# Kernel tuning notes

Hardware: AMD Instinct MI355X
Metric: run time of the kernel (lower is better)

The kernel has to match this reference:

```python
import jax, jax.numpy as jnp
import numpy as np

N_NODES = 100000
N_EDGES = 800000
N_GRAPHS = 256
IN_C = 96
HID = 96
OUT_C = 16


def setup_inputs() -> dict:
    key = jax.random.key(0)
    ks = jax.random.split(key, 10)
    x = jax.random.normal(ks[0], (N_NODES, IN_C), dtype=jnp.float32)
    edge_index = jax.random.randint(ks[1], (2, N_EDGES), 0, N_NODES, dtype=jnp.int64)
    batch = jnp.sort(jax.random.randint(ks[2], (N_NODES,), 0, N_GRAPHS, dtype=jnp.int64))
    def glorot(k, fan_in, fan_out):
        s = np.sqrt(6.0 / (fan_in + fan_out)).astype(np.float32)
        return jax.random.uniform(k, (fan_in, fan_out), minval=-s, maxval=s, dtype=jnp.float32)
    W1 = glorot(ks[3], IN_C, HID)
    W2 = glorot(ks[4], HID, HID)
    W3 = glorot(ks[5], HID, HID)
    Wlin = glorot(ks[6], HID, OUT_C)
    b1 = jnp.zeros((HID,), dtype=jnp.float32)
    b2 = jnp.zeros((HID,), dtype=jnp.float32)
    b3 = jnp.zeros((HID,), dtype=jnp.float32)
    return {"x": x, "edge_index": edge_index, "batch": batch,
            "W1": W1, "b1": b1, "W2": W2, "b2": b2, "W3": W3, "b3": b3, "Wlin": Wlin}


def _gcn_conv(x, W, b, src, dst):
    # PyG GCNConv(normalize=True): add self-loops, deg includes self-loop,
    # norm_ij = deg_i^{-1/2} * deg_j^{-1/2}; linear (no bias) then scatter-add; bias after.
    n = x.shape[0]
    deg = jnp.zeros((n,), dtype=x.dtype).at[dst].add(1.0) + 1.0  # +1 self-loop
    dinv = jax.lax.rsqrt(deg)
    h = x @ W                                   # [N, H]
    coef = dinv[src] * dinv[dst]                # [E]
    msg = h[src] * coef[:, None]                # [E, H] gather
    agg = jax.ops.segment_sum(msg, dst, num_segments=n)  # scatter-add
    agg = agg + h * (dinv * dinv)[:, None]      # self-loop contribution
    return agg + b


def reference(x, edge_index, batch, W1, b1, W2, b2, W3, b3, Wlin):
    src, dst = edge_index[0], edge_index[1]
    h = jax.nn.relu(_gcn_conv(x, W1, b1, src, dst))
    h = jax.nn.relu(_gcn_conv(h, W2, b2, src, dst))
    h = _gcn_conv(h, W3, b3, src, dst)
    # global mean pool over graphs
    sums = jax.ops.segment_sum(h, batch, num_segments=N_GRAPHS)
    counts = jax.ops.segment_sum(jnp.ones((h.shape[0],), dtype=h.dtype), batch, num_segments=N_GRAPHS)
    pooled = sums / jnp.maximum(counts, 1.0)[:, None]
    return pooled @ Wlin
```

## Files before the change

### kernel.cpp

```cpp
#include <hip/hip_runtime.h>

#define NN 100000
#define NE 800000
#define NG 256
#define CH 96
#define OC 16
#define NBLK 391
#define TM 128
#define WPAD 104

typedef __attribute__((ext_vector_type(8))) short bf16x8;
typedef __attribute__((ext_vector_type(4))) float f32x4;

__global__ __launch_bounds__(256) void k_hist(const int* __restrict__ dst,
                                              int* __restrict__ cnt,
                                              int* __restrict__ slot) {
    int e = blockIdx.x * 256 + threadIdx.x;
    slot[e] = atomicAdd(&cnt[dst[e]], 1);
}

__global__ __launch_bounds__(256) void k_scan1(const int* __restrict__ cnt,
                                               int* __restrict__ off,
                                               int* __restrict__ bsum) {
    __shared__ int sh[256];
    int t = threadIdx.x;
    int i = blockIdx.x * 256 + t;
    int v = (i < NN) ? cnt[i] : 0;
    sh[t] = v;
    __syncthreads();
    for (int d = 1; d < 256; d <<= 1) {
        int x = (t >= d) ? sh[t - d] : 0;
        __syncthreads();
        sh[t] += x;
        __syncthreads();
    }
    if (i < NN) off[i] = sh[t] - v;
    if (t == 255) bsum[blockIdx.x] = sh[255];
}

__global__ __launch_bounds__(512) void k_scan2(int* __restrict__ bsum,
                                               int* __restrict__ boff) {
    __shared__ int sh[512];
    int t = threadIdx.x;
    int v = (t < NBLK) ? bsum[t] : 0;
    sh[t] = v;
    __syncthreads();
    for (int d = 1; d < 512; d <<= 1) {
        int x = (t >= d) ? sh[t - d] : 0;
        __syncthreads();
        sh[t] += x;
        __syncthreads();
    }
    if (t < NBLK) boff[t] = sh[t] - v;
}

__global__ __launch_bounds__(256) void k_scan3(const int* __restrict__ cnt,
                                               int* __restrict__ off,
                                               const int* __restrict__ boff,
                                               float* __restrict__ dinv,
                                               const int* __restrict__ batch,
                                               int* __restrict__ goff) {
    int i = blockIdx.x * 256 + threadIdx.x;
    if (i >= NN) return;
    off[i] += boff[i >> 8];
    dinv[i] = rsqrtf((float)cnt[i] + 1.0f);
    int b = batch[i];
    int bp = (i > 0) ? batch[i - 1] : -1;
    for (int g = bp + 1; g <= b; g++) goff[g] = i;
    if (i == NN - 1)
        for (int g = b + 1; g <= NG; g++) goff[g] = NN;
}

__global__ __launch_bounds__(256) void k_build(const int* __restrict__ src,
                                               const int* __restrict__ dst,
                                               const int* __restrict__ off,
                                               const int* __restrict__ slot,
                                               const float* __restrict__ dinv,
                                               float2* __restrict__ packed) {
    int e = blockIdx.x * 256 + threadIdx.x;
    int s = src[e];
    int d = dst[e];
    packed[off[d] + slot[e]] = make_float2(__int_as_float(s), dinv[s] * dinv[d]);
}

__device__ __forceinline__ unsigned short f2bf(float x) {
    unsigned u = __float_as_uint(x);
    return (unsigned short)((u + 0x7fffu + ((u >> 16) & 1u)) >> 16);
}
__device__ __forceinline__ float bf2f(unsigned short h) {
    return __uint_as_float(((unsigned)h) << 16);
}

__device__ __forceinline__ void split8(const float4 a, const float4 b,
                                       bf16x8& hi, bf16x8& lo) {
    float v[8] = {a.x, a.y, a.z, a.w, b.x, b.y, b.z, b.w};
#pragma unroll
    for (int j = 0; j < 8; j++) {
        unsigned short h = f2bf(v[j]);
        hi[j] = (short)h;
        lo[j] = (short)f2bf(v[j] - bf2f(h));
    }
}

__global__ __launch_bounds__(256) void k_gemm96(const float* __restrict__ X,
                                                const float* __restrict__ W,
                                                unsigned short* __restrict__ H) {
    __shared__ unsigned short WtHi[CH * WPAD];
    __shared__ unsigned short WtLo[CH * WPAD];

    const int tid = threadIdx.x;
    const int n0 = blockIdx.x * TM;

    {
        const float4* W4 = reinterpret_cast<const float4*>(W);
#pragma unroll
        for (int i = 0; i < 9; i++) {
            int f4 = tid * 9 + i;
            int k = f4 / 24;
            int nn = (f4 - k * 24) * 4;
            float4 v = W4[f4];
            float vv[4] = {v.x, v.y, v.z, v.w};
#pragma unroll
            for (int e = 0; e < 4; e++) {
                unsigned short h = f2bf(vv[e]);
                WtHi[(nn + e) * WPAD + k] = h;
                WtLo[(nn + e) * WPAD + k] = f2bf(vv[e] - bf2f(h));
            }
        }
    }
    __syncthreads();

    const int lane = tid & 63;
    const int wave = tid >> 6;
    const int lrow = lane & 15;
    const int quad = lane >> 4;

    const float4* X4 = reinterpret_cast<const float4*>(X);

    f32x4 acc[2][6];
#pragma unroll
    for (int rt = 0; rt < 2; rt++)
#pragma unroll
        for (int ct = 0; ct < 6; ct++) acc[rt][ct] = (f32x4){0.f, 0.f, 0.f, 0.f};

    int arow[2];
#pragma unroll
    for (int rt = 0; rt < 2; rt++)
        arow[rt] = min(n0 + (wave * 2 + rt) * 16 + lrow, NN - 1);

#pragma unroll
    for (int kc = 0; kc < 3; kc++) {
        bf16x8 ahi[2], alo[2];
#pragma unroll
        for (int rt = 0; rt < 2; rt++) {
            int fo = (arow[rt] * CH + kc * 32 + quad * 8) >> 2;
            split8(X4[fo], X4[fo + 1], ahi[rt], alo[rt]);
        }
#pragma unroll
        for (int ct = 0; ct < 6; ct++) {
            int bo = (ct * 16 + lrow) * WPAD + kc * 32 + quad * 8;
            bf16x8 bhi = *reinterpret_cast<const bf16x8*>(&WtHi[bo]);
            bf16x8 blo = *reinterpret_cast<const bf16x8*>(&WtLo[bo]);
#pragma unroll
            for (int rt = 0; rt < 2; rt++) {
                acc[rt][ct] = __builtin_amdgcn_mfma_f32_16x16x32_bf16(
                    alo[rt], bhi, acc[rt][ct], 0, 0, 0);
                acc[rt][ct] = __builtin_amdgcn_mfma_f32_16x16x32_bf16(
                    ahi[rt], blo, acc[rt][ct], 0, 0, 0);
                acc[rt][ct] = __builtin_amdgcn_mfma_f32_16x16x32_bf16(
                    ahi[rt], bhi, acc[rt][ct], 0, 0, 0);
            }
        }
    }

#pragma unroll
    for (int rt = 0; rt < 2; rt++) {
        int rbase = n0 + (wave * 2 + rt) * 16 + quad * 4;
#pragma unroll
        for (int ct = 0; ct < 6; ct++) {
            int col = ct * 16 + lrow;
#pragma unroll
            for (int r = 0; r < 4; r++) {
                int row = rbase + r;
                if (row < NN) H[(size_t)row * CH + col] = f2bf(acc[rt][ct][r]);
            }
        }
    }
}

__device__ __forceinline__ float4 us4_to_f4(ushort4 u) {
    return make_float4(bf2f(u.x), bf2f(u.y), bf2f(u.z), bf2f(u.w));
}

template <bool RELU>
__global__ __launch_bounds__(256) void k_aggregate(const int* __restrict__ off,
                                                   const float2* __restrict__ packed,
                                                   const float* __restrict__ dinv,
                                                   const float* __restrict__ bias,
                                                   const unsigned short* __restrict__ H,
                                                   float* __restrict__ B) {
    int idx = blockIdx.x * 256 + threadIdx.x;
    int n = idx / 24;
    int c4 = idx - n * 24;
    int e0 = off[n];
    int e1 = (n + 1 < NN) ? off[n + 1] : NE;

    const ushort4* H4 = reinterpret_cast<const ushort4*>(H);
    float di = dinv[n];
    float d2 = di * di;
    float4 h = us4_to_f4(H4[(size_t)n * 24 + c4]);
    float4 bb = reinterpret_cast<const float4*>(bias)[c4];
    float4 acc = make_float4(h.x * d2 + bb.x, h.y * d2 + bb.y,
                             h.z * d2 + bb.z, h.w * d2 + bb.w);

    int e = e0;
    for (; e + 4 <= e1; e += 4) {
        float2 p0 = packed[e + 0];
        float2 p1 = packed[e + 1];
        float2 p2 = packed[e + 2];
        float2 p3 = packed[e + 3];
        float4 v0 = us4_to_f4(H4[(size_t)__float_as_int(p0.x) * 24 + c4]);
        float4 v1 = us4_to_f4(H4[(size_t)__float_as_int(p1.x) * 24 + c4]);
        float4 v2 = us4_to_f4(H4[(size_t)__float_as_int(p2.x) * 24 + c4]);
        float4 v3 = us4_to_f4(H4[(size_t)__float_as_int(p3.x) * 24 + c4]);
        acc.x += v0.x * p0.y + v1.x * p1.y + v2.x * p2.y + v3.x * p3.y;
        acc.y += v0.y * p0.y + v1.y * p1.y + v2.y * p2.y + v3.y * p3.y;
        acc.z += v0.z * p0.y + v1.z * p1.y + v2.z * p2.y + v3.z * p3.y;
        acc.w += v0.w * p0.y + v1.w * p1.y + v2.w * p2.y + v3.w * p3.y;
    }
    for (; e < e1; e++) {
        float2 pc = packed[e];
        float4 v = us4_to_f4(H4[(size_t)__float_as_int(pc.x) * 24 + c4]);
        acc.x += v.x * pc.y; acc.y += v.y * pc.y;
        acc.z += v.z * pc.y; acc.w += v.w * pc.y;
    }
    if (RELU) {
        acc.x = fmaxf(acc.x, 0.0f); acc.y = fmaxf(acc.y, 0.0f);
        acc.z = fmaxf(acc.z, 0.0f); acc.w = fmaxf(acc.w, 0.0f);
    }
    reinterpret_cast<float4*>(B)[(size_t)n * 24 + c4] = acc;
}

__global__ __launch_bounds__(384) void k_pool_linear(const int* __restrict__ goff,
                                                     const float* __restrict__ B,
                                                     const float* __restrict__ Wlin,
                                                     float* __restrict__ out) {
    __shared__ float4 sh[16][24];
    __shared__ float pooled[CH];
    int g = blockIdx.x;
    int t = threadIdx.x;
    int nl = t / 24;
    int c4 = t - nl * 24;
    int s = goff[g];
    int e = goff[g + 1];

    float4 acc = make_float4(0.f, 0.f, 0.f, 0.f);
    const float4* B4 = reinterpret_cast<const float4*>(B);
    for (int n = s + nl; n < e; n += 16) {
        float4 v = B4[(size_t)n * 24 + c4];
        acc.x += v.x; acc.y += v.y; acc.z += v.z; acc.w += v.w;
    }
    sh[nl][c4] = acc;
    __syncthreads();

    if (t < 24) {
        float4 r = make_float4(0.f, 0.f, 0.f, 0.f);
#pragma unroll
        for (int j = 0; j < 16; j++) {
            float4 v = sh[j][t];
            r.x += v.x; r.y += v.y; r.z += v.z; r.w += v.w;
        }
        float inv = 1.0f / fmaxf((float)(e - s), 1.0f);
        pooled[t * 4 + 0] = r.x * inv;
        pooled[t * 4 + 1] = r.y * inv;
        pooled[t * 4 + 2] = r.z * inv;
        pooled[t * 4 + 3] = r.w * inv;
    }
    __syncthreads();

    if (t < OC) {
        float a = 0.0f;
#pragma unroll 8
        for (int k = 0; k < CH; k++) a += pooled[k] * Wlin[k * OC + t];
        out[g * OC + t] = a;
    }
}

extern "C" void kernel_launch(void* const* d_in, const int* in_sizes, int n_in,
                              void* d_out, int out_size, void* d_ws, size_t ws_size,
                              hipStream_t stream) {
    const float* x = (const float*)d_in[0];
    const int* ei = (const int*)d_in[1];
    const int* src = ei;
    const int* dst = ei + NE;
    const int* batch = (const int*)d_in[2];
    const float* W1 = (const float*)d_in[3];
    const float* b1 = (const float*)d_in[4];
    const float* W2 = (const float*)d_in[5];
    const float* b2 = (const float*)d_in[6];
    const float* W3 = (const float*)d_in[7];
    const float* b3 = (const float*)d_in[8];
    const float* Wlin = (const float*)d_in[9];
    float* out = (float*)d_out;

    char* ws = (char*)d_ws;
    unsigned short* H = (unsigned short*)ws;  ws += (size_t)NN * CH * 2;
    float* B = (float*)ws;         ws += (size_t)NN * CH * 4;
    float2* packed = (float2*)ws;  ws += (size_t)NE * 8;
    float* dinv = (float*)ws;      ws += NN * 4;
    int* cnt = (int*)ws;           ws += NN * 4;
    int* off = (int*)ws;           ws += NN * 4;
    int* bsum = (int*)ws;          ws += 512 * 4;
    int* boff = (int*)ws;          ws += 512 * 4;
    int* goff = (int*)ws;          ws += (NG + 1) * 4;
    int* slot = (int*)B;

    hipMemsetAsync(cnt, 0, NN * 4, stream);
    k_hist<<<NE / 256, 256, 0, stream>>>(dst, cnt, slot);
    k_scan1<<<NBLK, 256, 0, stream>>>(cnt, off, bsum);
    k_scan2<<<1, 512, 0, stream>>>(bsum, boff);
    k_scan3<<<NBLK, 256, 0, stream>>>(cnt, off, boff, dinv, batch, goff);
    k_build<<<NE / 256, 256, 0, stream>>>(src, dst, off, slot, dinv, packed);

    const int gblk = (NN + TM - 1) / TM;

    k_gemm96<<<gblk, 256, 0, stream>>>(x, W1, H);
    k_aggregate<true><<<NN * 24 / 256, 256, 0, stream>>>(off, packed, dinv, b1, H, B);

    k_gemm96<<<gblk, 256, 0, stream>>>(B, W2, H);
    k_aggregate<true><<<NN * 24 / 256, 256, 0, stream>>>(off, packed, dinv, b2, H, B);

    k_gemm96<<<gblk, 256, 0, stream>>>(B, W3, H);
    k_aggregate<false><<<NN * 24 / 256, 256, 0, stream>>>(off, packed, dinv, b3, H, B);

    k_pool_linear<<<NG, 384, 0, stream>>>(goff, B, Wlin, out);
}
```

Before: 321.6 us.

## Replace scan with atomic offsets, pre-split weights once, pad edge tail loop

Replaces the three-kernel prefix scan with a single kernel that assigns per-node CSR offsets through an atomicAdd on a global counter, so segments land in arbitrary order and end offsets come from cnt. Weight bf16 hi/lo splitting and transposition move into a one-time prep kernel, and the GEMM blocks now just copy the pre-split weights into LDS, unpadded. The aggregation loop drops its scalar tail by padding the packed array and zeroing coefficients past the segment end. The cost is contended atomics in the offset kernel and edge segments that are no longer stored in node order, plus possible LDS bank conflicts from dropping the padding.

Measured after the change: 331.3 us. +3.0%, slower.

```diff
diff --git a/kernel.cpp b/kernel.cpp
--- a/kernel.cpp
+++ b/kernel.cpp
@@ -7,10 +7,30 @@
 #define OC 16
 #define NBLK 391
 #define TM 128
-#define WPAD 104
 
 typedef __attribute__((ext_vector_type(8))) short bf16x8;
 typedef __attribute__((ext_vector_type(4))) float f32x4;
+
+__device__ __forceinline__ unsigned short f2bf(float x) {
+    unsigned u = __float_as_uint(x);
+    return (unsigned short)((u + 0x7fffu + ((u >> 16) & 1u)) >> 16);
+}
+__device__ __forceinline__ float bf2f(unsigned short h) {
+    return __uint_as_float(((unsigned)h) << 16);
+}
+__device__ __forceinline__ void split8(const float4 a, const float4 b,
+                                       bf16x8& hi, bf16x8& lo) {
+    float v[8] = {a.x, a.y, a.z, a.w, b.x, b.y, b.z, b.w};
+#pragma unroll
+    for (int j = 0; j < 8; j++) {
+        unsigned short h = f2bf(v[j]);
+        hi[j] = (short)h;
+        lo[j] = (short)f2bf(v[j] - bf2f(h));
+    }
+}
+__device__ __forceinline__ float4 us4_to_f4(ushort4 u) {
+    return make_float4(bf2f(u.x), bf2f(u.y), bf2f(u.z), bf2f(u.w));
+}
 
 __global__ __launch_bounds__(256) void k_hist(const int* __restrict__ dst,
                                               int* __restrict__ cnt,
@@ -19,51 +39,17 @@
     slot[e] = atomicAdd(&cnt[dst[e]], 1);
 }
 
-__global__ __launch_bounds__(256) void k_scan1(const int* __restrict__ cnt,
-                                               int* __restrict__ off,
-                                               int* __restrict__ bsum) {
-    __shared__ int sh[256];
-    int t = threadIdx.x;
-    int i = blockIdx.x * 256 + t;
-    int v = (i < NN) ? cnt[i] : 0;
-    sh[t] = v;
-    __syncthreads();
-    for (int d = 1; d < 256; d <<= 1) {
-        int x = (t >= d) ? sh[t - d] : 0;
-        __syncthreads();
-        sh[t] += x;
-        __syncthreads();
-    }
-    if (i < NN) off[i] = sh[t] - v;
-    if (t == 255) bsum[blockIdx.x] = sh[255];
-}
-
-__global__ __launch_bounds__(512) void k_scan2(int* __restrict__ bsum,
-                                               int* __restrict__ boff) {
-    __shared__ int sh[512];
-    int t = threadIdx.x;
-    int v = (t < NBLK) ? bsum[t] : 0;
-    sh[t] = v;
-    __syncthreads();
-    for (int d = 1; d < 512; d <<= 1) {
-        int x = (t >= d) ? sh[t - d] : 0;
-        __syncthreads();
-        sh[t] += x;
-        __syncthreads();
-    }
-    if (t < NBLK) boff[t] = sh[t] - v;
-}
-
-__global__ __launch_bounds__(256) void k_scan3(const int* __restrict__ cnt,
-                                               int* __restrict__ off,
-                                               const int* __restrict__ boff,
-                                               float* __restrict__ dinv,
-                                               const int* __restrict__ batch,
-                                               int* __restrict__ goff) {
+__global__ __launch_bounds__(256) void k_offsets(const int* __restrict__ cnt,
+                                                 int* __restrict__ gtot,
+                                                 int* __restrict__ off,
+                                                 float* __restrict__ dinv,
+                                                 const int* __restrict__ batch,
+                                                 int* __restrict__ goff) {
     int i = blockIdx.x * 256 + threadIdx.x;
     if (i >= NN) return;
-    off[i] += boff[i >> 8];
-    dinv[i] = rsqrtf((float)cnt[i] + 1.0f);
+    int c = cnt[i];
+    off[i] = atomicAdd(gtot, c);
+    dinv[i] = rsqrtf((float)c + 1.0f);
     int b = batch[i];
     int bp = (i > 0) ? batch[i - 1] : -1;
     for (int g = bp + 1; g <= b; g++) goff[g] = i;
@@ -81,51 +67,46 @@
     int s = src[e];
     int d = dst[e];
     packed[off[d] + slot[e]] = make_float2(__int_as_float(s), dinv[s] * dinv[d]);
-}
-
-__device__ __forceinline__ unsigned short f2bf(float x) {
-    unsigned u = __float_as_uint(x);
-    return (unsigned short)((u + 0x7fffu + ((u >> 16) & 1u)) >> 16);
-}
-__device__ __forceinline__ float bf2f(unsigned short h) {
-    return __uint_as_float(((unsigned)h) << 16);
-}
-
-__device__ __forceinline__ void split8(const float4 a, const float4 b,
-                                       bf16x8& hi, bf16x8& lo) {
-    float v[8] = {a.x, a.y, a.z, a.w, b.x, b.y, b.z, b.w};
-#pragma unroll
-    for (int j = 0; j < 8; j++) {
-        unsigned short h = f2bf(v[j]);
-        hi[j] = (short)h;
-        lo[j] = (short)f2bf(v[j] - bf2f(h));
-    }
+    if (blockIdx.x == 0 && threadIdx.x < 8)
+        packed[NE + threadIdx.x] = make_float2(__int_as_float(0), 0.0f);
+}
+
+__global__ __launch_bounds__(256) void k_prep(const float* __restrict__ W1,
+                                              const float* __restrict__ W2,
+                                              const float* __restrict__ W3,
+                                              unsigned short* __restrict__ WH,
+                                              unsigned short* __restrict__ WL) {
+    int id = blockIdx.x * 256 + threadIdx.x;
+    if (id >= 3 * CH * CH) return;
+    int w = id / (CH * CH);
+    int r = id - w * CH * CH;
+    int k = r / CH;
+    int n = r - k * CH;
+    const float* Ws = (w == 0) ? W1 : (w == 1) ? W2 : W3;
+    float v = Ws[k * CH + n];
+    unsigned short h = f2bf(v);
+    WH[w * CH * CH + n * CH + k] = h;
+    WL[w * CH * CH + n * CH + k] = f2bf(v - bf2f(h));
 }
 
 __global__ __launch_bounds__(256) void k_gemm96(const float* __restrict__ X,
-                                                const float* __restrict__ W,
+                                                const unsigned short* __restrict__ WH,
+                                                const unsigned short* __restrict__ WL,
                                                 unsigned short* __restrict__ H) {
-    __shared__ unsigned short WtHi[CH * WPAD];
-    __shared__ unsigned short WtLo[CH * WPAD];
+    __shared__ __align__(16) unsigned short WsH[CH * CH];
+    __shared__ __align__(16) unsigned short WsL[CH * CH];
 
     const int tid = threadIdx.x;
     const int n0 = blockIdx.x * TM;
 
     {
-        const float4* W4 = reinterpret_cast<const float4*>(W);
-#pragma unroll
-        for (int i = 0; i < 9; i++) {
-            int f4 = tid * 9 + i;
-            int k = f4 / 24;
-            int nn = (f4 - k * 24) * 4;
-            float4 v = W4[f4];
-            float vv[4] = {v.x, v.y, v.z, v.w};
-#pragma unroll
-            for (int e = 0; e < 4; e++) {
-                unsigned short h = f2bf(vv[e]);
-                WtHi[(nn + e) * WPAD + k] = h;
-                WtLo[(nn + e) * WPAD + k] = f2bf(vv[e] - bf2f(h));
-            }
+        const uint4* sH = reinterpret_cast<const uint4*>(WH);
+        const uint4* sL = reinterpret_cast<const uint4*>(WL);
+        uint4* dH = reinterpret_cast<uint4*>(WsH);
+        uint4* dL = reinterpret_cast<uint4*>(WsL);
+        for (int i = tid; i < CH * CH / 8; i += 256) {
+            dH[i] = sH[i];
+            dL[i] = sL[i];
         }
     }
     __syncthreads();
@@ -158,9 +139,9 @@
         }
 #pragma unroll
         for (int ct = 0; ct < 6; ct++) {
-            int bo = (ct * 16 + lrow) * WPAD + kc * 32 + quad * 8;
-            bf16x8 bhi = *reinterpret_cast<const bf16x8*>(&WtHi[bo]);
-            bf16x8 blo = *reinterpret_cast<const bf16x8*>(&WtLo[bo]);
+            int bo = (ct * 16 + lrow) * CH + kc * 32 + quad * 8;
+            bf16x8 bhi = *reinterpret_cast<const bf16x8*>(&WsH[bo]);
+            bf16x8 blo = *reinterpret_cast<const bf16x8*>(&WsL[bo]);
 #pragma unroll
             for (int rt = 0; rt < 2; rt++) {
                 acc[rt][ct] = __builtin_amdgcn_mfma_f32_16x16x32_bf16(
@@ -188,12 +169,9 @@
     }
 }
 
-__device__ __forceinline__ float4 us4_to_f4(ushort4 u) {
-    return make_float4(bf2f(u.x), bf2f(u.y), bf2f(u.z), bf2f(u.w));
-}
-
 template <bool RELU>
 __global__ __launch_bounds__(256) void k_aggregate(const int* __restrict__ off,
+                                                   const int* __restrict__ cnt,
                                                    const float2* __restrict__ packed,
                                                    const float* __restrict__ dinv,
                                                    const float* __restrict__ bias,
@@ -203,7 +181,7 @@
     int n = idx / 24;
     int c4 = idx - n * 24;
     int e0 = off[n];
-    int e1 = (n + 1 < NN) ? off[n + 1] : NE;
+    int e1 = e0 + cnt[n];
 
     const ushort4* H4 = reinterpret_cast<const ushort4*>(H);
     float di = dinv[n];
@@ -213,26 +191,23 @@
     float4 acc = make_float4(h.x * d2 + bb.x, h.y * d2 + bb.y,
                              h.z * d2 + bb.z, h.w * d2 + bb.w);
 
-    int e = e0;
-    for (; e + 4 <= e1; e += 4) {
+    for (int e = e0; e < e1; e += 4) {
         float2 p0 = packed[e + 0];
         float2 p1 = packed[e + 1];
         float2 p2 = packed[e + 2];
         float2 p3 = packed[e + 3];
+        float c0 = p0.y;
+        float c1 = (e + 1 < e1) ? p1.y : 0.0f;
+        float c2 = (e + 2 < e1) ? p2.y : 0.0f;
+        float c3 = (e + 3 < e1) ? p3.y : 0.0f;
         float4 v0 = us4_to_f4(H4[(size_t)__float_as_int(p0.x) * 24 + c4]);
         float4 v1 = us4_to_f4(H4[(size_t)__float_as_int(p1.x) * 24 + c4]);
         float4 v2 = us4_to_f4(H4[(size_t)__float_as_int(p2.x) * 24 + c4]);
         float4 v3 = us4_to_f4(H4[(size_t)__float_as_int(p3.x) * 24 + c4]);
-        acc.x += v0.x * p0.y + v1.x * p1.y + v2.x * p2.y + v3.x * p3.y;
-        acc.y += v0.y * p0.y + v1.y * p1.y + v2.y * p2.y + v3.y * p3.y;
-        acc.z += v0.z * p0.y + v1.z * p1.y + v2.z * p2.y + v3.z * p3.y;
-        acc.w += v0.w * p0.y + v1.w * p1.y + v2.w * p2.y + v3.w * p3.y;
-    }
-    for (; e < e1; e++) {
-        float2 pc = packed[e];
-        float4 v = us4_to_f4(H4[(size_t)__float_as_int(pc.x) * 24 + c4]);
-        acc.x += v.x * pc.y; acc.y += v.y * pc.y;
-        acc.z += v.z * pc.y; acc.w += v.w * pc.y;
+        acc.x += v0.x * c0 + v1.x * c1 + v2.x * c2 + v3.x * c3;
+        acc.y += v0.y * c0 + v1.y * c1 + v2.y * c2 + v3.y * c3;
+        acc.z += v0.z * c0 + v1.z * c1 + v2.z * c2 + v3.z * c3;
+        acc.w += v0.w * c0 + v1.w * c1 + v2.w * c2 + v3.w * c3;
     }
     if (RELU) {
         acc.x = fmaxf(acc.x, 0.0f); acc.y = fmaxf(acc.y, 0.0f);
@@ -240,6 +215,7 @@
     }
     reinterpret_cast<float4*>(B)[(size_t)n * 24 + c4] = acc;
 }
+
 
 __global__ __launch_bounds__(384) void k_pool_linear(const int* __restrict__ goff,
                                                      const float* __restrict__ B,
@@ -304,34 +280,35 @@
     float* out = (float*)d_out;
 
     char* ws = (char*)d_ws;
-    unsigned short* H = (unsigned short*)ws;  ws += (size_t)NN * CH * 2;
-    float* B = (float*)ws;         ws += (size_t)NN * CH * 4;
-    float2* packed = (float2*)ws;  ws += (size_t)NE * 8;
-    float* dinv = (float*)ws;      ws += NN * 4;
-    int* cnt = (int*)ws;           ws += NN * 4;
-    int* off = (int*)ws;           ws += NN * 4;
-    int* bsum = (int*)ws;          ws += 512 * 4;
-    int* boff = (int*)ws;          ws += 512 * 4;
-    int* goff = (int*)ws;          ws += (NG + 1) * 4;
+    unsigned short* Ha = (unsigned short*)ws;  ws += (size_t)NN * CH * 2;
+    unsigned short* Hb = (unsigned short*)ws;  ws += (size_t)NN * CH * 2;
+    float* B = (float*)ws;          ws += (size_t)NN * CH * 4;
+    float2* packed = (float2*)ws;   ws += (size_t)(NE + 8) * 8;
+    unsigned short* WH = (unsigned short*)ws;  ws += 3 * CH * CH * 2;
+    unsigned short* WL = (unsigned short*)ws;  ws += 3 * CH * CH * 2;
+    float* dinv = (float*)ws;       ws += NN * 4;
+    int* off = (int*)ws;            ws += NN * 4;
+    int* goff = (int*)ws;           ws += 272 * 4;
+    int* cnt = (int*)ws;            ws += (NN + 4) * 4;
+    int* gtot = cnt + NN;
     int* slot = (int*)B;
 
-    hipMemsetAsync(cnt, 0, NN * 4, stream);
+    hipMemsetAsync(cnt, 0, (NN + 4) * 4, stream);
     k_hist<<<NE / 256, 256, 0, stream>>>(dst, cnt, slot);
-    k_scan1<<<NBLK, 256, 0, stream>>>(cnt, off, bsum);
-    k_scan2<<<1, 512, 0, stream>>>(bsum, boff);
-    k_scan3<<<NBLK, 256, 0, stream>>>(cnt, off, boff, dinv, batch, goff);
+    k_offsets<<<NBLK, 256, 0, stream>>>(cnt, gtot, off, dinv, batch, goff);
     k_build<<<NE / 256, 256, 0, stream>>>(src, dst, off, slot, dinv, packed);
+    k_prep<<<(3 * CH * CH + 255) / 256, 256, 0, stream>>>(W1, W2, W3, WH, WL);
 
     const int gblk = (NN + TM - 1) / TM;
 
-    k_gemm96<<<gblk, 256, 0, stream>>>(x, W1, H);
-    k_aggregate<true><<<NN * 24 / 256, 256, 0, stream>>>(off, packed, dinv, b1, H, B);
-
-    k_gemm96<<<gblk, 256, 0, stream>>>(B, W2, H);
-    k_aggregate<true><<<NN * 24 / 256, 256, 0, stream>>>(off, packed, dinv, b2, H, B);
-
-    k_gemm96<<<gblk, 256, 0, stream>>>(B, W3, H);
-    k_aggregate<false><<<NN * 24 / 256, 256, 0, stream>>>(off, packed, dinv, b3, H, B);
+    k_gemm96<<<gblk, 256, 0, stream>>>(x, WH, WL, Ha);
+    k_aggregate<true><<<NN * 24 / 256, 256, 0, stream>>>(off, cnt, packed, dinv, b1, Ha, B);
+
+    k_gemm96<<<gblk, 256, 0, stream>>>(B, WH + CH * CH, WL + CH * CH, Hb);
+    k_aggregate<true><<<NN * 24 / 256, 256, 0, stream>>>(off, cnt, packed, dinv, b2, Hb, B);
+
+    k_gemm96<<<gblk, 256, 0, stream>>>(B, WH + 2 * CH * CH, WL + 2 * CH * CH, Ha);
+    k_aggregate<false><<<NN * 24 / 256, 256, 0, stream>>>(off, cnt, packed, dinv, b3, Ha, B);
 
     k_pool_linear<<<NG, 384, 0, stream>>>(goff, B, Wlin, out);
 }
```
